# Performance work log

Measured on AMD Instinct MI355X. Metric: run time of the kernel, lower is better.

The kernel has to match this reference:

```python
import jax, jax.numpy as jnp
from jax import lax
import numpy as np

GWS = (2, 7, 7)          # grid_window_size
NUM_HEADS = 4
DIM = 256
HEAD_DIM = DIM // NUM_HEADS
SCALE = HEAD_DIM ** -0.5


def _rel_index(ws):
    d, h, w = ws
    coords = np.stack(np.meshgrid(np.arange(d), np.arange(h), np.arange(w), indexing='ij')).reshape(3, -1)
    rel = (coords[:, :, None] - coords[:, None, :]).transpose(1, 2, 0)
    rel[:, :, 0] += d - 1
    rel[:, :, 1] += h - 1
    rel[:, :, 2] += w - 1
    rel[:, :, 0] *= (2 * h - 1) * (2 * w - 1)
    rel[:, :, 1] *= (2 * w - 1)
    return rel.sum(-1)

RPI = jnp.asarray(_rel_index(GWS))  # (98, 98) int, constant buffer


def _ln(x, w, b, eps=1e-5):
    m = x.mean(-1, keepdims=True)
    v = ((x - m) ** 2).mean(-1, keepdims=True)
    return (x - m) * lax.rsqrt(v + eps) * w + b


def _attention(x, qkv_w, proj_w, proj_b, bias_table):
    # x: (num_windows, N, C); qkv has no bias in the original (qkv_bias=False)
    Bw, N, C = x.shape
    qkv = (x @ qkv_w.T).reshape(Bw, N, 3, NUM_HEADS, HEAD_DIM).transpose(2, 0, 3, 1, 4)
    q, k, v = qkv[0] * SCALE, qkv[1], qkv[2]
    scores = jnp.einsum('bhnd,bhmd->bhnm', q, k)
    bias = bias_table[RPI.reshape(-1)].reshape(N, N, NUM_HEADS).transpose(2, 0, 1)
    a = jax.nn.softmax(scores + bias[None], axis=-1)
    out = jnp.einsum('bhnm,bhmd->bhnd', a, v).transpose(0, 2, 1, 3).reshape(Bw, N, C)
    return out @ proj_w.T + proj_b


def _window_partition(x):
    B, D, H, W, C = x.shape
    d, h, w = GWS
    x = x.reshape(B, D // d, d, H // h, h, W // w, w, C).transpose(0, 1, 3, 5, 2, 4, 6, 7)
    return x.reshape(-1, d * h * w, C)


def _window_reverse(win, B, D, H, W):
    d, h, w = GWS
    x = win.reshape(B, D // d, H // h, W // w, d, h, w, -1).transpose(0, 1, 4, 2, 5, 3, 6, 7)
    return x.reshape(B, D, H, W, -1)


def _grid_partition(x):
    B, D, H, W, C = x.shape
    d, h, w = GWS
    x = x.reshape(B, d, D // d, h, H // h, w, W // w, C).transpose(0, 2, 4, 6, 1, 3, 5, 7)
    return x.reshape(-1, d * h * w, C)


def _grid_reverse(g, B, D, H, W):
    d, h, w = GWS
    x = g.reshape(B, D // d, H // h, W // w, d, h, w, -1).transpose(0, 4, 1, 5, 2, 6, 3, 7)
    return x.reshape(B, D, H, W, -1)


def _conv3d(x, w, b):
    y = lax.conv_general_dilated(x, w, (1, 1, 1), 'SAME',
                                 dimension_numbers=('NCDHW', 'OIDHW', 'NCDHW'))
    return y + b[None, :, None, None, None]


def _leaky(x):
    return jnp.where(x >= 0, x, 0.01 * x)


def setup_inputs() -> dict:
    key = jax.random.key(0)
    ks = jax.random.split(key, 12)
    B, D, H, W = 2, 8, 56, 56
    dim = DIM
    TBL = (2 * GWS[0] - 1) * (2 * GWS[1] - 1) * (2 * GWS[2] - 1)  # 507
    p = lambda k, s: jax.random.normal(k, s, jnp.float32) * 0.02
    return {
        'input': jax.random.normal(ks[0], (B, dim, D, H, W), jnp.float32),
        'n1w': jnp.ones((dim,), jnp.float32), 'n1b': jnp.zeros((dim,), jnp.float32),
        'n2w': jnp.ones((dim,), jnp.float32), 'n2b': jnp.zeros((dim,), jnp.float32),
        'wqkv': p(ks[1], (3 * dim, dim)),
        'wprojw': p(ks[2], (dim, dim)), 'wprojb': jnp.zeros((dim,), jnp.float32),
        'wbias': p(ks[3], (TBL, NUM_HEADS)),
        'gqkv': p(ks[4], (3 * dim, dim)),
        'gprojw': p(ks[5], (dim, dim)), 'gprojb': jnp.zeros((dim,), jnp.float32),
        'gbias': p(ks[6], (TBL, NUM_HEADS)),
        'f1c1w': p(ks[7], (128, 128, 3, 3, 3)), 'f1c1b': jnp.zeros((128,), jnp.float32),
        'f1c2w': p(ks[8], (128, 128, 3, 3, 3)), 'f1c2b': jnp.zeros((128,), jnp.float32),
        'g1c1w': p(ks[9], (128, 128, 3, 3, 3)), 'g1c1b': jnp.zeros((128,), jnp.float32),
        'g1c2w': p(ks[10], (128, 128, 3, 3, 3)), 'g1c2b': jnp.zeros((128,), jnp.float32),
    }


def reference(input, n1w, n1b, n2w, n2b, wqkv, wprojw, wprojb, wbias,
              gqkv, gprojw, gprojb, gbias,
              f1c1w, f1c1b, f1c2w, f1c2b, g1c1w, g1c1b, g1c2w, g1c2b):
    B, C, D, H, W = input.shape
    x = input.transpose(0, 2, 3, 4, 1)  # b d h w c
    x = _ln(x, n1w, n1b)
    pd = (GWS[0] - D % GWS[0]) % GWS[0]
    ph = (GWS[1] - H % GWS[1]) % GWS[1]
    pw = (GWS[2] - W % GWS[2]) % GWS[2]
    if pd or ph or pw:
        x = jnp.pad(x, ((0, 0), (0, pd), (0, ph), (0, pw), (0, 0)))
    Dp, Hp, Wp = D + pd, H + ph, W + pw
    # block (window) attention
    win = _window_partition(x)
    win = _attention(win, wqkv, wprojw, wprojb, wbias)
    xw = _window_reverse(win, B, Dp, Hp, Wp)
    # grid attention
    y = _ln(xw, n2w, n2b)
    g = _grid_partition(y)
    g = _attention(g, gqkv, gprojw, gprojb, gbias)
    y = _grid_reverse(g, B, Dp, Hp, Wp) + xw
    if pd or ph or pw:
        y = y[:, :D, :H, :W, :]
    y = y.transpose(0, 4, 1, 2, 3)  # b c d h w
    s = input + y
    # reversible conv block: split 256 -> 128/128
    x1, x2 = s[:, :C // 2], s[:, C // 2:]
    y1 = x1 + _conv3d(_leaky(_conv3d(x2, f1c1w, f1c1b)), f1c2w, f1c2b)
    y2 = x2 + _conv3d(_leaky(_conv3d(y1, g1c1w, g1c1b)), g1c2w, g1c2b)
    return jnp.concatenate([y1, y2], axis=1)
```

## Files before the change

kernel.cpp:

```cpp
#include <hip/hip_runtime.h>
#include <stdint.h>


typedef unsigned short u16;
typedef __attribute__((ext_vector_type(8))) short short8;
typedef __attribute__((ext_vector_type(4))) float f32x4;

#define TOK   50176
#define CH    256
#define SPAT  25088
#define PLANE 3136

__device__ __forceinline__ float b2f(u16 u) {
    union { uint32_t i; float f; } v; v.i = ((uint32_t)u) << 16; return v.f;
}
__device__ __forceinline__ u16 f2b(float f) {
    union { float f; uint32_t i; } v; v.f = f;
    uint32_t i = v.i;
    uint32_t r = i + 0x7FFFu + ((i >> 16) & 1u);
    return (u16)(r >> 16);
}

__global__ __launch_bounds__(256) void ln1_kernel(
    const float* __restrict__ x, const float* __restrict__ w,
    const float* __restrict__ bsh, u16* __restrict__ out)
{
    int t = blockIdx.x * 256 + threadIdx.x;
    int b = t / SPAT, sp = t % SPAT;
    const float* px = x + (size_t)b * CH * SPAT + sp;
    float s = 0.f, ss = 0.f;
    for (int c = 0; c < CH; c++) { float v = px[(size_t)c * SPAT]; s += v; ss += v * v; }
    float mean = s * (1.0f / CH);
    float var  = ss * (1.0f / CH) - mean * mean;
    float rstd = rsqrtf(var + 1e-5f);
    u16* po = out + (size_t)t * CH;
    for (int c = 0; c < CH; c++) {
        float v = (px[(size_t)c * SPAT] - mean) * rstd * w[c] + bsh[c];
        po[c] = f2b(v);
    }
}

__global__ __launch_bounds__(256) void ln2_kernel(
    const u16* __restrict__ x, const float* __restrict__ w,
    const float* __restrict__ bsh, u16* __restrict__ out)
{
    int wave = threadIdx.x >> 6, lane = threadIdx.x & 63;
    int t = blockIdx.x * 4 + wave;
    const u16* px = x + (size_t)t * CH + lane * 4;
    ushort4 v4 = *(const ushort4*)px;
    float v0 = b2f(v4.x), v1 = b2f(v4.y), v2 = b2f(v4.z), v3 = b2f(v4.w);
    float s = v0 + v1 + v2 + v3;
    float ss = v0*v0 + v1*v1 + v2*v2 + v3*v3;
    for (int o = 32; o > 0; o >>= 1) {
        s  += __shfl_xor(s,  o, 64);
        ss += __shfl_xor(ss, o, 64);
    }
    float mean = s * (1.0f / CH);
    float rstd = rsqrtf(ss * (1.0f / CH) - mean * mean + 1e-5f);
    float4 w4 = *(const float4*)(w + lane * 4);
    float4 b4 = *(const float4*)(bsh + lane * 4);
    ushort4 o4;
    o4.x = f2b((v0 - mean) * rstd * w4.x + b4.x);
    o4.y = f2b((v1 - mean) * rstd * w4.y + b4.y);
    o4.z = f2b((v2 - mean) * rstd * w4.z + b4.z);
    o4.w = f2b((v3 - mean) * rstd * w4.w + b4.w);
    *(ushort4*)(out + (size_t)t * CH + lane * 4) = o4;
}

__global__ __launch_bounds__(256) void gemm_mfma_kernel(
    const u16* __restrict__ A, const float* __restrict__ B,
    const float* __restrict__ bias, const u16* __restrict__ res,
    u16* __restrict__ C, int Nout)
{
    __shared__ u16 sAg[128][72];
    __shared__ u16 sBg[128][72];
    int tid = threadIdx.x;
    int m0 = blockIdx.x * 128, n0g = blockIdx.y * 128;
    int lane = tid & 63, wv = tid >> 6;
    int quad = lane >> 4, l15 = lane & 15;
    int mw = (wv & 1) * 64, nw = (wv >> 1) * 64;

    f32x4 zz = {0.f, 0.f, 0.f, 0.f};
    f32x4 acc[4][4];
    #pragma unroll
    for (int i = 0; i < 4; i++)
        #pragma unroll
        for (int j = 0; j < 4; j++) acc[i][j] = zz;

    for (int kc = 0; kc < 256; kc += 64) {
        __syncthreads();
        #pragma unroll
        for (int i = 0; i < 4; i++) {
            int unit = tid + i * 256;
            int row = unit >> 3, k8 = (unit & 7) << 3;
            *(uint4*)&sAg[row][k8] = *(const uint4*)(A + (size_t)(m0 + row) * 256 + kc + k8);
        }
        #pragma unroll
        for (int i = 0; i < 8; i++) {
            int unit = tid + i * 256;
            int row = unit >> 4, k4 = (unit & 15) << 2;
            float4 v = *(const float4*)(B + (size_t)(n0g + row) * 256 + kc + k4);
            ushort4 p;
            p.x = f2b(v.x); p.y = f2b(v.y); p.z = f2b(v.z); p.w = f2b(v.w);
            *(ushort4*)&sBg[row][k4] = p;
        }
        __syncthreads();
        #pragma unroll
        for (int kk = 0; kk < 2; kk++) {
            short8 afr[4], bfr[4];
            #pragma unroll
            for (int mt = 0; mt < 4; mt++)
                afr[mt] = *(const short8*)&sAg[mw + mt*16 + l15][kk*32 + quad*8];
            #pragma unroll
            for (int nt = 0; nt < 4; nt++)
                bfr[nt] = *(const short8*)&sBg[nw + nt*16 + l15][kk*32 + quad*8];
            #pragma unroll
            for (int mt = 0; mt < 4; mt++)
                #pragma unroll
                for (int nt = 0; nt < 4; nt++)
                    acc[mt][nt] = __builtin_amdgcn_mfma_f32_16x16x32_bf16(
                        afr[mt], bfr[nt], acc[mt][nt], 0, 0, 0);
        }
    }

    #pragma unroll
    for (int nt = 0; nt < 4; nt++) {
        int n = n0g + nw + nt*16 + l15;
        float bv = bias ? bias[n] : 0.f;
        #pragma unroll
        for (int mt = 0; mt < 4; mt++) {
            int m = m0 + mw + mt*16 + quad*4;
            #pragma unroll
            for (int r = 0; r < 4; r++) {
                float v = acc[mt][nt][r] + bv;
                size_t off = (size_t)(m + r) * Nout + n;
                if (res) v += b2f(res[off]);
                C[off] = f2b(v);
            }
        }
    }
}

__global__ __launch_bounds__(256) void attn_mfma_kernel(
    const u16* __restrict__ qkv, const float* __restrict__ btab,
    u16* __restrict__ outp, int mode)
{
    __shared__ u16 sKV[8704];
    __shared__ u16 sS[112][136];
    __shared__ float sBias[507];
    __shared__ int sTok[112];
    __shared__ int sEnc[112];
    __shared__ float sInv[112];

    int g = blockIdx.x, head = blockIdx.y, tid = threadIdx.x;
    int b  = g >> 8;
    int gd = (g >> 6) & 3, gh = (g >> 3) & 7, gw = g & 7;

    int lane = tid & 63, wv = tid >> 6;
    int quad = lane >> 4, l15 = lane & 15;
    int mts[2] = {wv, wv + 4};

    if (tid < 112) {
        int t = tid;
        int i = t / 49, r = t % 49, j = r / 7, k = r % 7;
        sEnc[tid] = i * 169 + j * 13 + k;
        int tokv = 0;
        if (t < 98) {
            int d, h, w;
            if (mode == 0) { d = gd*2 + i; h = gh*7 + j; w = gw*7 + k; }
            else           { d = i*4 + gd; h = j*8 + gh; w = k*8 + gw; }
            tokv = ((b*8 + d)*56 + h)*56 + w;
        }
        sTok[tid] = tokv;
    }
    for (int idx = tid; idx < 507; idx += 256) sBias[idx] = btab[idx * 4 + head];
    __syncthreads();

    for (int idx = tid; idx < 112 * 8; idx += 256) {
        int row = idx >> 3, c8 = (idx & 7) << 3;
        uint4 v = {0u, 0u, 0u, 0u};
        if (row < 98)
            v = *(const uint4*)(qkv + (size_t)sTok[row] * 768 + 256 + head * 64 + c8);
        *(uint4*)&sKV[row * 72 + c8] = v;
    }
    __syncthreads();

    short8 qf[2][2];
    #pragma unroll
    for (int mi = 0; mi < 2; mi++) {
        int mt = mts[mi];
        #pragma unroll
        for (int ks = 0; ks < 2; ks++) {
            short8 v;
            #pragma unroll
            for (int j = 0; j < 8; j++) v[j] = 0;
            int row = mt * 16 + l15;
            if (mt < 7 && row < 98)
                v = *(const short8*)(qkv + (size_t)sTok[row] * 768 + head * 64 + ks * 32 + quad * 8);
            qf[mi][ks] = v;
        }
    }

    f32x4 zz = {0.f, 0.f, 0.f, 0.f};
    #pragma unroll
    for (int mi = 0; mi < 2; mi++) {
        int mt = mts[mi];
        if (mt >= 7) continue;
        for (int nt = 0; nt < 7; nt++) {
            f32x4 acc = zz;
            acc = __builtin_amdgcn_mfma_f32_16x16x32_bf16(
                qf[mi][0], *(const short8*)&sKV[(nt*16 + l15) * 72 + quad*8], acc, 0, 0, 0);
            acc = __builtin_amdgcn_mfma_f32_16x16x32_bf16(
                qf[mi][1], *(const short8*)&sKV[(nt*16 + l15) * 72 + 32 + quad*8], acc, 0, 0, 0);
            int n = nt * 16 + l15;
            int en = (n < 98) ? sEnc[n] : 0;
            #pragma unroll
            for (int r = 0; r < 4; r++) {
                int m = mt * 16 + quad * 4 + r;
                float v;
                if (n < 98) {
                    int em = sEnc[m < 98 ? m : 97];
                    v = acc[r] * 0.125f + sBias[em - en + 253];
                } else v = -1e30f;
                sS[m][n] = f2b(v);
            }
        }
    }
    __syncthreads();

    for (int idx = tid; idx < 64 * 30; idx += 256) {
        int c = idx / 30, t = 98 + idx % 30;
        sKV[c * 136 + t] = 0;
    }
    for (int idx = tid; idx < 98 * 8; idx += 256) {
        int tok = idx >> 3, c8 = (idx & 7) << 3;
        uint4 v = *(const uint4*)(qkv + (size_t)sTok[tok] * 768 + 512 + head * 64 + c8);
        const u16* pv = (const u16*)&v;
        #pragma unroll
        for (int j = 0; j < 8; j++) sKV[(c8 + j) * 136 + tok] = pv[j];
    }

    {
        int row = tid >> 1, half = tid & 1;
        if (row < 112) {
            #pragma unroll
            for (int j = 0; j < 8; j++) sS[row][112 + half * 8 + j] = 0;
        }
        if (row < 98) {
            int c0 = half * 49;
            float mx = -1e30f;
            for (int j = 0; j < 49; j++) mx = fmaxf(mx, b2f(sS[row][c0 + j]));
            mx = fmaxf(mx, __shfl_xor(mx, 1, 64));
            float sum = 0.f;
            for (int j = 0; j < 49; j++) {
                float e = __expf(b2f(sS[row][c0 + j]) - mx);
                sum += e;
                sS[row][c0 + j] = f2b(e);
            }
            sum += __shfl_xor(sum, 1, 64);
            if (half == 0) sInv[row] = 1.0f / sum;
        }
    }
    __syncthreads();

    f32x4 po[2][4];
    #pragma unroll
    for (int mi = 0; mi < 2; mi++)
        #pragma unroll
        for (int nt = 0; nt < 4; nt++) po[mi][nt] = zz;

    #pragma unroll
    for (int mi = 0; mi < 2; mi++) {
        int mt = mts[mi];
        if (mt >= 7) continue;
        for (int ks = 0; ks < 4; ks++) {
            short8 ap = *(const short8*)&sS[mt*16 + l15][ks*32 + quad*8];
            #pragma unroll
            for (int nt = 0; nt < 4; nt++) {
                short8 bv = *(const short8*)&sKV[(nt*16 + l15) * 136 + ks*32 + quad*8];
                po[mi][nt] = __builtin_amdgcn_mfma_f32_16x16x32_bf16(ap, bv, po[mi][nt], 0, 0, 0);
            }
        }
    }

    #pragma unroll
    for (int mi = 0; mi < 2; mi++) {
        int mt = mts[mi];
        if (mt >= 7) continue;
        #pragma unroll
        for (int r = 0; r < 4; r++) {
            int m = mt * 16 + quad * 4 + r;
            if (m >= 98) continue;
            float inv = sInv[m];
            u16* dst = outp + (size_t)sTok[m] * 256 + head * 64 + l15;
            #pragma unroll
            for (int nt = 0; nt < 4; nt++)
                dst[nt * 16] = f2b(po[mi][nt][r] * inv);
        }
    }
}

__global__ __launch_bounds__(256) void ssplit_cl_kernel(
    const float* __restrict__ inp, const u16* __restrict__ y,
    u16* __restrict__ s1, u16* __restrict__ s2)
{
    __shared__ float sT[64][65];
    int t0 = blockIdx.x * 64;
    int b = t0 / SPAT, sp0 = t0 % SPAT;
    int tid = threadIdx.x;
    for (int cg = 0; cg < 4; cg++) {
        __syncthreads();
        #pragma unroll
        for (int i = 0; i < 16; i++) {
            int unit = tid + i * 256;
            int cl = unit >> 6, spl = unit & 63;
            sT[spl][cl] = inp[((size_t)(b * 256 + cg * 64 + cl)) * SPAT + sp0 + spl];
        }
        __syncthreads();
        int spl = tid >> 2, c16 = (tid & 3) * 16;
        int tok = t0 + spl;
        const u16* yp = y + (size_t)tok * 256 + cg * 64 + c16;
        int cbase = cg * 64 + c16;
        u16* dst = (cbase < 128) ? (s1 + (size_t)tok * 128 + cbase)
                                 : (s2 + (size_t)tok * 128 + cbase - 128);
        #pragma unroll
        for (int j = 0; j < 16; j++) {
            float v = sT[spl][c16 + j] + b2f(yp[j]);
            dst[j] = f2b(v);
        }
    }
}

__global__ __launch_bounds__(256) void convw_kernel(
    const float* __restrict__ w, u16* __restrict__ o)
{
    int e = blockIdx.x * 256 + threadIdx.x;
    int tap = e >> 14;
    int r = e & 16383;
    int kk = r >> 12;
    int nt = (r >> 9) & 7;
    int quad = (r >> 7) & 3;
    int l15 = (r >> 3) & 15;
    int j = r & 7;
    int oc = nt * 16 + l15;
    int ic = kk * 32 + quad * 8 + j;
    o[e] = f2b(w[(size_t)(oc * 128 + ic) * 27 + tap]);
}

__global__ __launch_bounds__(256, 3) void conv_mfma_kernel(
    const u16* __restrict__ in_cl,
    const u16* __restrict__ wtf,
    const float* __restrict__ bias,
    const u16* __restrict__ res_cl,
    u16* __restrict__ out_cl,
    float* __restrict__ out_f32,
    int oc_base, int leaky)
{
    __shared__ u16 sA[2][8192];
    __shared__ int sD[64], sHH[64], sWW[64];

    int tid = threadIdx.x;
    int t0 = blockIdx.x * 64;
    int b = t0 / SPAT, sp0 = t0 % SPAT;

    if (tid < 64) {
        int sp = sp0 + tid;
        int d = sp / PLANE, r = sp % PLANE;
        sD[tid] = d; sHH[tid] = r / 56; sWW[tid] = r % 56;
    }
    __syncthreads();

    int lane = tid & 63, wv = tid >> 6;
    int quad = lane >> 4, l15 = lane & 15;
    int n0 = wv * 32;

    int u_l15[4], u_kq[4], u_m[4];
    #pragma unroll
    for (int i = 0; i < 4; i++) {
        int unit = tid + i * 256;
        int mtkk = unit >> 6;
        int mt = mtkk & 3;
        u_m[i]  = mt * 16 + (unit & 15);
        u_kq[i] = ((mtkk >> 2) * 32 + ((unit >> 4) & 3) * 8);
        u_l15[i] = unit;
    }

    f32x4 zz = {0.f, 0.f, 0.f, 0.f};
    f32x4 acc[4][2];
    #pragma unroll
    for (int i = 0; i < 4; i++) { acc[i][0] = zz; acc[i][1] = zz; }

    uint4 pre[4];

    #define STAGE_REGS(TAP)                                                    \
    {                                                                          \
        int kd = (TAP) / 9 - 1, kh = ((TAP) / 3) % 3 - 1, kw = (TAP) % 3 - 1;  \
        _Pragma("unroll")                                                      \
        for (int i = 0; i < 4; i++) {                                          \
            int m = u_m[i];                                                    \
            int dd = sD[m] + kd, hh = sHH[m] + kh, ww = sWW[m] + kw;           \
            uint4 v = {0u, 0u, 0u, 0u};                                        \
            if ((unsigned)dd < 8u && (unsigned)hh < 56u && (unsigned)ww < 56u) \
                v = *(const uint4*)(in_cl +                                    \
                    ((size_t)(b * 8 + dd) * PLANE + hh * 56 + ww) * 128 + u_kq[i]); \
            pre[i] = v;                                                        \
        }                                                                      \
    }

    STAGE_REGS(0);
    #pragma unroll
    for (int i = 0; i < 4; i++) *(uint4*)&sA[0][u_l15[i] * 8] = pre[i];
    __syncthreads();

    for (int tap = 0; tap < 27; tap++) {
        int cur = tap & 1;
        if (tap < 26) STAGE_REGS(tap + 1);

        const u16* wb = wtf + tap * 16384;
        #pragma unroll
        for (int kk = 0; kk < 4; kk++) {
            short8 afr[4], bfr[2];
            #pragma unroll
            for (int mt = 0; mt < 4; mt++)
                afr[mt] = *(const short8*)&sA[cur][((kk*4 + mt)*64 + lane) * 8];
            #pragma unroll
            for (int nt = 0; nt < 2; nt++)
                bfr[nt] = *(const short8*)(wb + ((kk*8 + n0/16 + nt)*64 + lane) * 8);
            #pragma unroll
            for (int mt = 0; mt < 4; mt++)
                #pragma unroll
                for (int nt = 0; nt < 2; nt++)
                    acc[mt][nt] = __builtin_amdgcn_mfma_f32_16x16x32_bf16(
                        afr[mt], bfr[nt], acc[mt][nt], 0, 0, 0);
        }

        if (tap < 26) {
            #pragma unroll
            for (int i = 0; i < 4; i++) *(uint4*)&sA[cur ^ 1][u_l15[i] * 8] = pre[i];
        }
        __syncthreads();
    }
    #undef STAGE_REGS

    #pragma unroll
    for (int nt = 0; nt < 2; nt++) {
        int oc = n0 + nt*16 + l15;
        float bv = bias[oc];
        #pragma unroll
        for (int mt = 0; mt < 4; mt++) {
            int m = mt*16 + quad*4;
            #pragma unroll
            for (int r = 0; r < 4; r++) {
                float v = acc[mt][nt][r] + bv;
                if (leaky) v = (v >= 0.f) ? v : 0.01f * v;
                if (res_cl) v += b2f(res_cl[(size_t)(t0 + m + r) * 128 + oc]);
                acc[mt][nt][r] = v;
            }
        }
    }

    if (out_cl) {
        #pragma unroll
        for (int mt = 0; mt < 4; mt++) {
            int m = mt*16 + quad*4;
            #pragma unroll
            for (int nt = 0; nt < 2; nt++) {
                int oc = n0 + nt*16 + l15;
                #pragma unroll
                for (int r = 0; r < 4; r++)
                    out_cl[(size_t)(t0 + m + r) * 128 + oc] = f2b(acc[mt][nt][r]);
            }
        }
    }

    if (out_f32) {
        __syncthreads();
        float* sT = (float*)&sA[0][0];
        #pragma unroll
        for (int mt = 0; mt < 4; mt++) {
            int m = mt*16 + quad*4;
            #pragma unroll
            for (int nt = 0; nt < 2; nt++) {
                int oc = n0 + nt*16 + l15;
                #pragma unroll
                for (int r = 0; r < 4; r++)
                    sT[oc * 64 + ((m + r + oc) & 63)] = acc[mt][nt][r];
            }
        }
        __syncthreads();
        int oc = tid >> 1, half = tid & 1;
        size_t obase = ((size_t)b * 256 + oc_base + oc) * SPAT + sp0 + half * 32;
        const float* row = &sT[oc * 64];
        for (int j = 0; j < 32; j++) {
            int m = half * 32 + j;
            out_f32[obase + j] = row[(m + oc) & 63];
        }
    }
}

extern "C" void kernel_launch(void* const* d_in, const int* in_sizes, int n_in,
                              void* d_out, int out_size, void* d_ws, size_t ws_size,
                              hipStream_t stream)
{
    const float* input  = (const float*)d_in[0];
    const float* n1w    = (const float*)d_in[1];
    const float* n1b    = (const float*)d_in[2];
    const float* n2w    = (const float*)d_in[3];
    const float* n2b    = (const float*)d_in[4];
    const float* wqkv   = (const float*)d_in[5];
    const float* wprojw = (const float*)d_in[6];
    const float* wprojb = (const float*)d_in[7];
    const float* wbias  = (const float*)d_in[8];
    const float* gqkv   = (const float*)d_in[9];
    const float* gprojw = (const float*)d_in[10];
    const float* gprojb = (const float*)d_in[11];
    const float* gbias  = (const float*)d_in[12];
    const float* f1c1w  = (const float*)d_in[13];
    const float* f1c1b  = (const float*)d_in[14];
    const float* f1c2w  = (const float*)d_in[15];
    const float* f1c2b  = (const float*)d_in[16];
    const float* g1c1w  = (const float*)d_in[17];
    const float* g1c1b  = (const float*)d_in[18];
    const float* g1c2w  = (const float*)d_in[19];
    const float* g1c2b  = (const float*)d_in[20];

    char* ws = (char*)d_ws;
    u16* xln   = (u16*)(ws);
    u16* qkv   = (u16*)(ws + 25690112);
    u16* attnb = (u16*)(ws + 102760448);
    u16* xw    = (u16*)(ws + 128450560);
    u16* y  = xln;
    u16* s1   = qkv;
    u16* s2   = (u16*)(ws + 25690112 + 12845056);
    u16* tb   = (u16*)(ws + 25690112 + 25690112);
    u16* y1cl = (u16*)(ws + 25690112 + 38535168);
    u16* cw0  = (u16*)(ws + 25690112 + 51380224);
    u16* cw1  = cw0 + 442368;
    u16* cw2  = cw1 + 442368;
    u16* cw3  = cw2 + 442368;

    float* outp = (float*)d_out;

    ln1_kernel<<<196, 256, 0, stream>>>(input, n1w, n1b, xln);
    gemm_mfma_kernel<<<dim3(392, 6), 256, 0, stream>>>(xln, wqkv, nullptr, nullptr, qkv, 768);
    attn_mfma_kernel<<<dim3(512, 4), 256, 0, stream>>>(qkv, wbias, attnb, 0);
    gemm_mfma_kernel<<<dim3(392, 2), 256, 0, stream>>>(attnb, wprojw, wprojb, nullptr, xw, 256);
    ln2_kernel<<<12544, 256, 0, stream>>>(xw, n2w, n2b, xln);
    gemm_mfma_kernel<<<dim3(392, 6), 256, 0, stream>>>(xln, gqkv, nullptr, nullptr, qkv, 768);
    attn_mfma_kernel<<<dim3(512, 4), 256, 0, stream>>>(qkv, gbias, attnb, 1);
    gemm_mfma_kernel<<<dim3(392, 2), 256, 0, stream>>>(attnb, gprojw, gprojb, xw, y, 256);
    ssplit_cl_kernel<<<784, 256, 0, stream>>>(input, y, s1, s2);
    convw_kernel<<<1728, 256, 0, stream>>>(f1c1w, cw0);
    convw_kernel<<<1728, 256, 0, stream>>>(f1c2w, cw1);
    convw_kernel<<<1728, 256, 0, stream>>>(g1c1w, cw2);
    convw_kernel<<<1728, 256, 0, stream>>>(g1c2w, cw3);
    conv_mfma_kernel<<<784, 256, 0, stream>>>(s2, cw0, f1c1b, nullptr, tb, nullptr, 0, 1);
    conv_mfma_kernel<<<784, 256, 0, stream>>>(tb, cw1, f1c2b, s1, y1cl, outp, 0, 0);
    conv_mfma_kernel<<<784, 256, 0, stream>>>(y1cl, cw2, g1c1b, nullptr, tb, nullptr, 0, 1);
    conv_mfma_kernel<<<784, 256, 0, stream>>>(tb, cw3, g1c2b, s2, nullptr, outp, 128, 0);
}
```

Baseline: 854.8 us.

## Load conv A-fragments directly from global memory, dropping LDS staging

The 3D conv kernel no longer stages the input tile in double-buffered shared memory. Each lane now computes per-tap addresses and loads its MFMA A-fragments straight from global memory. Out-of-bounds taps point to a zeroed 256-byte pad placed after each buffer, so no masking is needed. This removes the per-tap LDS stores and __syncthreads and raises the launch-bounds occupancy hint from 3 to 4. The cost is uncoalesced, redundant global or L2 reads across waves, since each of the four waves reloads the same A data, plus three extra memset calls and a rearranged workspace layout.

New measurement: 1.311 ms. +53.4%, slower.

```diff
diff --git a/kernel.cpp b/kernel.cpp
--- a/kernel.cpp
+++ b/kernel.cpp
@@ -347,7 +347,7 @@
     o[e] = f2b(w[(size_t)(oc * 128 + ic) * 27 + tap]);
 }
 
-__global__ __launch_bounds__(256, 3) void conv_mfma_kernel(
+__global__ __launch_bounds__(256, 4) void conv_mfma_kernel(
     const u16* __restrict__ in_cl,
     const u16* __restrict__ wtf,
     const float* __restrict__ bias,
@@ -356,65 +356,47 @@
     float* __restrict__ out_f32,
     int oc_base, int leaky)
 {
-    __shared__ u16 sA[2][8192];
-    __shared__ int sD[64], sHH[64], sWW[64];
+    __shared__ float sT[128][64];
 
     int tid = threadIdx.x;
     int t0 = blockIdx.x * 64;
     int b = t0 / SPAT, sp0 = t0 % SPAT;
 
-    if (tid < 64) {
-        int sp = sp0 + tid;
-        int d = sp / PLANE, r = sp % PLANE;
-        sD[tid] = d; sHH[tid] = r / 56; sWW[tid] = r % 56;
-    }
-    __syncthreads();
-
     int lane = tid & 63, wv = tid >> 6;
     int quad = lane >> 4, l15 = lane & 15;
     int n0 = wv * 32;
-
-    int u_l15[4], u_kq[4], u_m[4];
-    #pragma unroll
-    for (int i = 0; i < 4; i++) {
-        int unit = tid + i * 256;
-        int mtkk = unit >> 6;
-        int mt = mtkk & 3;
-        u_m[i]  = mt * 16 + (unit & 15);
-        u_kq[i] = ((mtkk >> 2) * 32 + ((unit >> 4) & 3) * 8);
-        u_l15[i] = unit;
-    }
+    int nbase = wv * 2;
+
+    int d_m[4], h_m[4], w_m[4];
+    int lin_m[4];
+    #pragma unroll
+    for (int mt = 0; mt < 4; mt++) {
+        int sp = sp0 + mt * 16 + l15;
+        int d = sp / PLANE; int rr = sp % PLANE;
+        d_m[mt] = d; h_m[mt] = rr / 56; w_m[mt] = rr % 56;
+        lin_m[mt] = t0 + mt * 16 + l15;
+    }
+    const int icb = quad * 8;
+    const int ZOFF = TOK * 128 + icb;
 
     f32x4 zz = {0.f, 0.f, 0.f, 0.f};
     f32x4 acc[4][2];
     #pragma unroll
     for (int i = 0; i < 4; i++) { acc[i][0] = zz; acc[i][1] = zz; }
 
-    uint4 pre[4];
-
-    #define STAGE_REGS(TAP)                                                    \
-    {                                                                          \
-        int kd = (TAP) / 9 - 1, kh = ((TAP) / 3) % 3 - 1, kw = (TAP) % 3 - 1;  \
-        _Pragma("unroll")                                                      \
-        for (int i = 0; i < 4; i++) {                                          \
-            int m = u_m[i];                                                    \
-            int dd = sD[m] + kd, hh = sHH[m] + kh, ww = sWW[m] + kw;           \
-            uint4 v = {0u, 0u, 0u, 0u};                                        \
-            if ((unsigned)dd < 8u && (unsigned)hh < 56u && (unsigned)ww < 56u) \
-                v = *(const uint4*)(in_cl +                                    \
-                    ((size_t)(b * 8 + dd) * PLANE + hh * 56 + ww) * 128 + u_kq[i]); \
-            pre[i] = v;                                                        \
-        }                                                                      \
-    }
-
-    STAGE_REGS(0);
-    #pragma unroll
-    for (int i = 0; i < 4; i++) *(uint4*)&sA[0][u_l15[i] * 8] = pre[i];
-    __syncthreads();
-
     for (int tap = 0; tap < 27; tap++) {
-        int cur = tap & 1;
-        if (tap < 26) STAGE_REGS(tap + 1);
+        int kd = tap / 9 - 1;
+        int r9 = tap % 9;
+        int kh = r9 / 3 - 1, kw = r9 % 3 - 1;
+        int tapoff = kd * PLANE + kh * 56 + kw;
+
+        int aoff[4];
+        #pragma unroll
+        for (int mt = 0; mt < 4; mt++) {
+            int dd = d_m[mt] + kd, hh = h_m[mt] + kh, ww = w_m[mt] + kw;
+            bool ok = ((unsigned)dd < 8u) & ((unsigned)hh < 56u) & ((unsigned)ww < 56u);
+            aoff[mt] = ok ? ((lin_m[mt] + tapoff) * 128 + icb) : ZOFF;
+        }
 
         const u16* wb = wtf + tap * 16384;
         #pragma unroll
@@ -422,10 +404,10 @@
             short8 afr[4], bfr[2];
             #pragma unroll
             for (int mt = 0; mt < 4; mt++)
-                afr[mt] = *(const short8*)&sA[cur][((kk*4 + mt)*64 + lane) * 8];
+                afr[mt] = *(const short8*)(in_cl + aoff[mt] + kk * 32);
             #pragma unroll
             for (int nt = 0; nt < 2; nt++)
-                bfr[nt] = *(const short8*)(wb + ((kk*8 + n0/16 + nt)*64 + lane) * 8);
+                bfr[nt] = *(const short8*)(wb + ((kk*8 + nbase + nt)*64 + lane) * 8);
             #pragma unroll
             for (int mt = 0; mt < 4; mt++)
                 #pragma unroll
@@ -433,14 +415,7 @@
                     acc[mt][nt] = __builtin_amdgcn_mfma_f32_16x16x32_bf16(
                         afr[mt], bfr[nt], acc[mt][nt], 0, 0, 0);
         }
-
-        if (tap < 26) {
-            #pragma unroll
-            for (int i = 0; i < 4; i++) *(uint4*)&sA[cur ^ 1][u_l15[i] * 8] = pre[i];
-        }
-        __syncthreads();
-    }
-    #undef STAGE_REGS
+    }
 
     #pragma unroll
     for (int nt = 0; nt < 2; nt++) {
@@ -474,8 +449,6 @@
     }
 
     if (out_f32) {
-        __syncthreads();
-        float* sT = (float*)&sA[0][0];
         #pragma unroll
         for (int mt = 0; mt < 4; mt++) {
             int m = mt*16 + quad*4;
@@ -484,13 +457,13 @@
                 int oc = n0 + nt*16 + l15;
                 #pragma unroll
                 for (int r = 0; r < 4; r++)
-                    sT[oc * 64 + ((m + r + oc) & 63)] = acc[mt][nt][r];
+                    sT[oc][(m + r + oc) & 63] = acc[mt][nt][r];
             }
         }
         __syncthreads();
         int oc = tid >> 1, half = tid & 1;
         size_t obase = ((size_t)b * 256 + oc_base + oc) * SPAT + sp0 + half * 32;
-        const float* row = &sT[oc * 64];
+        const float* row = &sT[oc][0];
         for (int j = 0; j < 32; j++) {
             int m = half * 32 + j;
             out_f32[obase + j] = row[(m + oc) & 63];
@@ -530,11 +503,11 @@
     u16* attnb = (u16*)(ws + 102760448);
     u16* xw    = (u16*)(ws + 128450560);
     u16* y  = xln;
-    u16* s1   = qkv;
-    u16* s2   = (u16*)(ws + 25690112 + 12845056);
-    u16* tb   = (u16*)(ws + 25690112 + 25690112);
-    u16* y1cl = (u16*)(ws + 25690112 + 38535168);
-    u16* cw0  = (u16*)(ws + 25690112 + 51380224);
+    u16* s1   = (u16*)(ws + 25690112);
+    u16* s2   = (u16*)(ws + 38535168);
+    u16* tb   = (u16*)(ws + 51380480);
+    u16* y1cl = (u16*)(ws + 64225792);
+    u16* cw0  = (u16*)(ws + 77071104);
     u16* cw1  = cw0 + 442368;
     u16* cw2  = cw1 + 442368;
     u16* cw3  = cw2 + 442368;
@@ -550,6 +523,9 @@
     attn_mfma_kernel<<<dim3(512, 4), 256, 0, stream>>>(qkv, gbias, attnb, 1);
     gemm_mfma_kernel<<<dim3(392, 2), 256, 0, stream>>>(attnb, gprojw, gprojb, xw, y, 256);
     ssplit_cl_kernel<<<784, 256, 0, stream>>>(input, y, s1, s2);
+    hipMemsetAsync((char*)s2   + 12845056, 0, 256, stream);
+    hipMemsetAsync((char*)tb   + 12845056, 0, 256, stream);
+    hipMemsetAsync((char*)y1cl + 12845056, 0, 256, stream);
     convw_kernel<<<1728, 256, 0, stream>>>(f1c1w, cw0);
     convw_kernel<<<1728, 256, 0, stream>>>(f1c2w, cw1);
     convw_kernel<<<1728, 256, 0, stream>>>(g1c1w, cw2);
```
